# Optimization experiments

Measured on AMD Instinct MI355X. Metric: run time of the kernel, lower is better.

## Reference

```python
import jax, jax.numpy as jnp
import numpy as np

C = 1000      # num_classes
U = 10        # proxies_per_class
D = 512       # feature_dim
B = 4096      # batch
ALPHA = 32.0
DELTA = 0.1


def _l2norm(x, axis=-1):
    return x / jnp.linalg.norm(x, axis=axis, keepdims=True).clip(1e-12)


def setup_inputs() -> dict:
    key = jax.random.key(0)
    k1, k2, k3 = jax.random.split(key, 3)
    features = jax.random.normal(k1, (B, D), dtype=jnp.float32)
    labels = jax.random.randint(k2, (B,), 0, C)
    # proxies are initialized to row-normalized gaussians (as in __init__)
    proxies = _l2norm(jax.random.normal(k3, (C * U, D), dtype=jnp.float32))
    return {"features": features, "labels": labels, "proxies": proxies}


def reference(features, labels, proxies):
    # proxy_class_ids: [C*U], class id of each proxy
    class_ids = jnp.repeat(jnp.arange(C), U)

    x = _l2norm(features)          # [B, D]
    p = _l2norm(proxies)           # [P, D], P = C*U
    sim = x @ p.T                  # [B, P]

    # ---- infer_logits, agg='soft', tau=1 ----
    s = sim.reshape(B, C, U)       # per-class proxy similarities
    w = jax.nn.softmax(s, axis=2)
    logits = jnp.sum(w * s, axis=2)  # [B, C], tau=1 so no extra scaling

    # ---- _compute_proxy_loss (Proxy-Anchor) ----
    sim_t = sim.T                                         # [P, B]
    pos_mask = labels[None, :] == class_ids[:, None]      # [P, B]
    neg_inf = jnp.finfo(jnp.float32).min
    z_pos = jnp.where(pos_mask, -ALPHA * (sim_t - DELTA), neg_inf)
    z_neg = jnp.where(pos_mask, neg_inf, ALPHA * (sim_t + DELTA))
    lse_pos = jax.nn.logsumexp(z_pos, axis=1)             # [P]
    lse_neg = jax.nn.logsumexp(z_neg, axis=1)             # [P]
    pos_term = jax.nn.softplus(lse_pos)
    neg_term = jax.nn.softplus(lse_neg)
    has_pos = pos_mask.any(axis=1)
    pos_loss = jnp.where(has_pos, pos_term, 0.0).sum() / jnp.maximum(
        has_pos.sum(), 1).astype(jnp.float32)
    neg_loss = neg_term.mean()
    proxy_loss = pos_loss + neg_loss

    return logits, proxy_loss
```

## Files before the change

kernel.cpp:

```cpp
#include <hip/hip_runtime.h>
#include <hip/hip_bf16.h>

#define C_CLS   1000
#define U_PX    10
#define D_DIM   512
#define B_BATCH 4096
#define P_PX    (C_CLS * U_PX)
#define ALPHA_F 32.0f
#define DELTA_F 0.1f

#define BM 256
#define BN 80
#define BK 64
#define SIMP 84

#define A_OFF   0
#define B_OFF   32768
#define SMEM_SZ 43008

typedef __attribute__((ext_vector_type(8))) short bf16x8;
typedef __attribute__((ext_vector_type(4))) float f32x4;

typedef __attribute__((address_space(1))) const void gv_t;
typedef __attribute__((address_space(3))) void lv_t;

__device__ __forceinline__ void gload_lds16(const void* g, void* lds) {
    __builtin_amdgcn_global_load_lds((gv_t*)g, (lv_t*)lds, 16, 0, 0);
}

__device__ __forceinline__ unsigned int f2bf(float f) {
    union { float f; unsigned u; } c; c.f = f;
    unsigned u = c.u;
    return (u + 0x7FFF + ((u >> 16) & 1)) >> 16;
}

__global__ __launch_bounds__(256) void norm_rows_kernel(const float* __restrict__ feat,
                                                        const float* __restrict__ prox,
                                                        unsigned int* __restrict__ xout,
                                                        unsigned int* __restrict__ pout) {
    const int wid  = threadIdx.x >> 6;
    const int lane = threadIdx.x & 63;
    int row = blockIdx.x * 4 + wid;
    const float* in;
    unsigned int* out;
    if (row < B_BATCH) { in = feat + (size_t)row * D_DIM;   out = xout + (size_t)row * (D_DIM / 2); }
    else { row -= B_BATCH; in = prox + (size_t)row * D_DIM; out = pout + (size_t)row * (D_DIM / 2); }
    const float4 v0 = reinterpret_cast<const float4*>(in)[lane * 2];
    const float4 v1 = reinterpret_cast<const float4*>(in)[lane * 2 + 1];
    float ss = v0.x*v0.x + v0.y*v0.y + v0.z*v0.z + v0.w*v0.w
             + v1.x*v1.x + v1.y*v1.y + v1.z*v1.z + v1.w*v1.w;
    #pragma unroll
    for (int off = 1; off < 64; off <<= 1) ss += __shfl_xor(ss, off, 64);
    const float inv = 1.0f / fmaxf(sqrtf(ss), 1e-12f);
    uint4 o;
    o.x = f2bf(v0.x * inv) | (f2bf(v0.y * inv) << 16);
    o.y = f2bf(v0.z * inv) | (f2bf(v0.w * inv) << 16);
    o.z = f2bf(v1.x * inv) | (f2bf(v1.y * inv) << 16);
    o.w = f2bf(v1.z * inv) | (f2bf(v1.w * inv) << 16);
    *reinterpret_cast<uint4*>(out + lane * 4) = o;
}

__global__ __launch_bounds__(256, 3) void fused_gemm_kernel(
    const unsigned short* __restrict__ xbf,
    const unsigned short* __restrict__ pbf,
    const int*            __restrict__ labels,
    float*                __restrict__ logits,
    double*               __restrict__ pos_sum,
    double*               __restrict__ neg_sum)
{
    __shared__ __align__(16) char smem[SMEM_SZ];
    __shared__ int lab_lds[BM];

    const int t    = threadIdx.x;
    const int m0   = blockIdx.x * BM;
    const int n0   = blockIdx.y * BN;
    const int wid  = t >> 6;
    const int lane = t & 63;
    const int l15  = lane & 15;
    const int kgrp = lane >> 4;

    if (t < BM) lab_lds[t] = labels[m0 + t];

    const int srow = lane >> 3;
    const int scol = (lane & 7) ^ srow;

    const int koff0 = ((kgrp    ) ^ (l15 & 7)) << 4;
    const int koff1 = ((kgrp + 4) ^ (l15 & 7)) << 4;

    f32x4 acc[4][5];
    #pragma unroll
    for (int m = 0; m < 4; ++m)
        #pragma unroll
        for (int n = 0; n < 5; ++n) acc[m][n] = (f32x4){0.f, 0.f, 0.f, 0.f};

    for (int ks = 0; ks < D_DIM / BK; ++ks) {
        const int kbase = ks * BK;
        #pragma unroll
        for (int c = wid; c < 32; c += 4)
            gload_lds16(xbf + (size_t)(m0 + c * 8 + srow) * D_DIM + kbase + scol * 8,
                        smem + A_OFF + c * 1024);
        for (int c = wid; c < 10; c += 4)
            gload_lds16(pbf + (size_t)(n0 + c * 8 + srow) * D_DIM + kbase + scol * 8,
                        smem + B_OFF + c * 1024);
        __syncthreads();
        #pragma unroll
        for (int kk8 = 0; kk8 < 2; ++kk8) {
            const int koff = kk8 ? koff1 : koff0;
            bf16x8 b[5];
            #pragma unroll
            for (int n = 0; n < 5; ++n)
                b[n] = *reinterpret_cast<const bf16x8*>(smem + B_OFF + (n * 16 + l15) * 128 + koff);
            #pragma unroll
            for (int m = 0; m < 4; ++m) {
                const bf16x8 a = *reinterpret_cast<const bf16x8*>(
                    smem + A_OFF + (wid * 64 + m * 16 + l15) * 128 + koff);
                #pragma unroll
                for (int n = 0; n < 5; ++n)
                    acc[m][n] = __builtin_amdgcn_mfma_f32_16x16x32_bf16(a, b[n], acc[m][n], 0, 0, 0);
            }
        }
        __syncthreads();
    }

    {
        int labv[16];
        #pragma unroll
        for (int m = 0; m < 4; ++m)
            #pragma unroll
            for (int r = 0; r < 4; ++r)
                labv[m * 4 + r] = lab_lds[wid * 64 + m * 16 + kgrp * 4 + r];
        #pragma unroll
        for (int n = 0; n < 5; ++n) {
            const int col = n * 16 + l15;
            const int cls = (n0 + col) / U_PX;
            float pos = 0.f, neg = 0.f;
            #pragma unroll
            for (int m = 0; m < 4; ++m)
                #pragma unroll
                for (int r = 0; r < 4; ++r) {
                    const float s = acc[m][n][r];
                    const bool isp = (labv[m * 4 + r] == cls);
                    const float e = __expf(isp ? (-ALPHA_F * (s - DELTA_F))
                                               : ( ALPHA_F * (s + DELTA_F)));
                    if (isp) pos += e; else neg += e;
                }
            pos += __shfl_xor(pos, 16, 64); pos += __shfl_xor(pos, 32, 64);
            neg += __shfl_xor(neg, 16, 64); neg += __shfl_xor(neg, 32, 64);
            if (lane < 16) {
                atomicAdd(&neg_sum[n0 + col], (double)neg);
                if (pos != 0.f) atomicAdd(&pos_sum[n0 + col], (double)pos);
            }
        }
    }

    float* simw = reinterpret_cast<float*>(smem) + wid * (16 * SIMP);
    #pragma unroll
    for (int m = 0; m < 4; ++m) {
        #pragma unroll
        for (int n = 0; n < 5; ++n)
            #pragma unroll
            for (int r = 0; r < 4; ++r)
                simw[(kgrp * 4 + r) * SIMP + n * 16 + l15] = acc[m][n][r];
        #pragma unroll
        for (int it = 0; it < 2; ++it) {
            const int j   = lane + it * 64;
            const int r   = j >> 3;
            const int c   = j & 7;
            const float* s = simw + r * SIMP + c * U_PX;
            float wsum = 0.f, wssum = 0.f;
            #pragma unroll
            for (int u = 0; u < U_PX; ++u) {
                const float sv = s[u];
                const float e = __expf(sv);
                wsum += e; wssum += e * sv;
            }
            logits[(size_t)(m0 + wid * 64 + m * 16 + r) * C_CLS + (n0 / U_PX + c)] = wssum / wsum;
        }
        __builtin_amdgcn_s_waitcnt(0);
    }
}

__global__ __launch_bounds__(1024) void finalize_kernel(
    const int*    __restrict__ labels,
    const double* __restrict__ pos_sum,
    const double* __restrict__ neg_sum,
    float*        __restrict__ out_loss)
{
    __shared__ int    hist[C_CLS];
    __shared__ double sp[1024], sn[1024];
    __shared__ int    sc[1024];
    const int t = threadIdx.x;
    for (int i = t; i < C_CLS; i += 1024) hist[i] = 0;
    __syncthreads();
    for (int i = t; i < B_BATCH; i += 1024) atomicAdd(&hist[labels[i]], 1);
    __syncthreads();
    double pAcc = 0.0, nAcc = 0.0; int cnt = 0;
    for (int p = t; p < P_PX; p += 1024) {
        nAcc += log1p(neg_sum[p]);
        if (hist[p / U_PX] > 0) { pAcc += log1p(pos_sum[p]); cnt++; }
    }
    sp[t] = pAcc; sn[t] = nAcc; sc[t] = cnt;
    __syncthreads();
    for (int s = 512; s > 0; s >>= 1) {
        if (t < s) { sp[t] += sp[t + s]; sn[t] += sn[t + s]; sc[t] += sc[t + s]; }
        __syncthreads();
    }
    if (t == 0)
        out_loss[0] = (float)(sp[0] / (double)max(sc[0], 1) + sn[0] / (double)P_PX);
}

extern "C" void kernel_launch(void* const* d_in, const int* in_sizes, int n_in,
                              void* d_out, int out_size, void* d_ws, size_t ws_size,
                              hipStream_t stream) {
    const float* features = (const float*)d_in[0];
    const int*   labels   = (const int*)d_in[1];
    const float* proxies  = (const float*)d_in[2];
    float* out = (float*)d_out;

    char* ws = (char*)d_ws;
    unsigned short* xbf = (unsigned short*)ws;
    unsigned short* pbf = (unsigned short*)(ws + (size_t)B_BATCH * D_DIM * 2);
    double* pos_sum = (double*)(ws + (size_t)(B_BATCH + P_PX) * D_DIM * 2);
    double* neg_sum = pos_sum + P_PX;

    hipMemsetAsync(pos_sum, 0, 2 * P_PX * sizeof(double), stream);

    norm_rows_kernel<<<(B_BATCH + P_PX) / 4, 256, 0, stream>>>(
        features, proxies, (unsigned int*)xbf, (unsigned int*)pbf);

    fused_gemm_kernel<<<dim3(B_BATCH / BM, P_PX / BN), 256, 0, stream>>>(
        xbf, pbf, labels, out, pos_sum, neg_sum);

    finalize_kernel<<<1, 1024, 0, stream>>>(labels, pos_sum, neg_sum,
                                            out + (size_t)B_BATCH * C_CLS);
}
```

Baseline: 106.6 us.

## Double-buffer GEMM LDS tiles with smaller blocks and parallelize loss finalize

The fused GEMM kernel now uses 128-row tiles with two waves per block and two LDS buffers, so the global-to-LDS loads for the next K step are issued before the MFMA work on the current one. This is meant to overlap memory traffic with compute and to launch more, smaller blocks. The single-block finalize kernel is replaced by a multi-block partial reduction using wave shuffles and double atomics, followed by a tiny final kernel. The label histogram is dropped in favour of testing whether pos_sum is nonzero, which assumes the exp terms never underflow to zero.

```diff
diff --git a/kernel.cpp b/kernel.cpp
--- a/kernel.cpp
+++ b/kernel.cpp
@@ -9,14 +9,15 @@
 #define ALPHA_F 32.0f
 #define DELTA_F 0.1f
 
-#define BM 256
+#define BM 128
 #define BN 80
 #define BK 64
 #define SIMP 84
 
-#define A_OFF   0
-#define B_OFF   32768
-#define SMEM_SZ 43008
+#define A_OFF      0
+#define B_OFF      16384
+#define BUF_STRIDE 26624
+#define SMEM_SZ    (2 * BUF_STRIDE)
 
 typedef __attribute__((ext_vector_type(8))) short bf16x8;
 typedef __attribute__((ext_vector_type(4))) float f32x4;
@@ -60,7 +61,7 @@
     *reinterpret_cast<uint4*>(out + lane * 4) = o;
 }
 
-__global__ __launch_bounds__(256, 3) void fused_gemm_kernel(
+__global__ __launch_bounds__(128, 3) void fused_gemm_kernel(
     const unsigned short* __restrict__ xbf,
     const unsigned short* __restrict__ pbf,
     const int*            __restrict__ labels,
@@ -79,7 +80,7 @@
     const int l15  = lane & 15;
     const int kgrp = lane >> 4;
 
-    if (t < BM) lab_lds[t] = labels[m0 + t];
+    lab_lds[t] = labels[m0 + t];
 
     const int srow = lane >> 3;
     const int scol = (lane & 7) ^ srow;
@@ -93,27 +94,37 @@
         #pragma unroll
         for (int n = 0; n < 5; ++n) acc[m][n] = (f32x4){0.f, 0.f, 0.f, 0.f};
 
+    #define STAGE(ks_, buf_)                                                            \
+        do {                                                                            \
+            const int kb_ = (ks_) * BK;                                                 \
+            char* base_ = smem + (buf_) * BUF_STRIDE;                                   \
+            _Pragma("unroll")                                                           \
+            for (int c = wid; c < 16; c += 2)                                           \
+                gload_lds16(xbf + (size_t)(m0 + c * 8 + srow) * D_DIM + kb_ + scol * 8, \
+                            base_ + A_OFF + c * 1024);                                  \
+            _Pragma("unroll")                                                           \
+            for (int c = wid; c < 10; c += 2)                                           \
+                gload_lds16(pbf + (size_t)(n0 + c * 8 + srow) * D_DIM + kb_ + scol * 8, \
+                            base_ + B_OFF + c * 1024);                                  \
+        } while (0)
+
+    STAGE(0, 0);
+    __syncthreads();
+
     for (int ks = 0; ks < D_DIM / BK; ++ks) {
-        const int kbase = ks * BK;
-        #pragma unroll
-        for (int c = wid; c < 32; c += 4)
-            gload_lds16(xbf + (size_t)(m0 + c * 8 + srow) * D_DIM + kbase + scol * 8,
-                        smem + A_OFF + c * 1024);
-        for (int c = wid; c < 10; c += 4)
-            gload_lds16(pbf + (size_t)(n0 + c * 8 + srow) * D_DIM + kbase + scol * 8,
-                        smem + B_OFF + c * 1024);
-        __syncthreads();
+        const char* base = smem + (ks & 1) * BUF_STRIDE;
+        if (ks < D_DIM / BK - 1) STAGE(ks + 1, (ks + 1) & 1);
         #pragma unroll
         for (int kk8 = 0; kk8 < 2; ++kk8) {
             const int koff = kk8 ? koff1 : koff0;
             bf16x8 b[5];
             #pragma unroll
             for (int n = 0; n < 5; ++n)
-                b[n] = *reinterpret_cast<const bf16x8*>(smem + B_OFF + (n * 16 + l15) * 128 + koff);
+                b[n] = *reinterpret_cast<const bf16x8*>(smem + (ks & 1) * BUF_STRIDE + B_OFF + (n * 16 + l15) * 128 + koff);
             #pragma unroll
             for (int m = 0; m < 4; ++m) {
                 const bf16x8 a = *reinterpret_cast<const bf16x8*>(
-                    smem + A_OFF + (wid * 64 + m * 16 + l15) * 128 + koff);
+                    base + A_OFF + (wid * 64 + m * 16 + l15) * 128 + koff);
                 #pragma unroll
                 for (int n = 0; n < 5; ++n)
                     acc[m][n] = __builtin_amdgcn_mfma_f32_16x16x32_bf16(a, b[n], acc[m][n], 0, 0, 0);
@@ -180,33 +191,38 @@
     }
 }
 
-__global__ __launch_bounds__(1024) void finalize_kernel(
-    const int*    __restrict__ labels,
+__global__ __launch_bounds__(256) void finalize_partial_kernel(
     const double* __restrict__ pos_sum,
     const double* __restrict__ neg_sum,
-    float*        __restrict__ out_loss)
+    double*       __restrict__ accum)
 {
-    __shared__ int    hist[C_CLS];
-    __shared__ double sp[1024], sn[1024];
-    __shared__ int    sc[1024];
-    const int t = threadIdx.x;
-    for (int i = t; i < C_CLS; i += 1024) hist[i] = 0;
-    __syncthreads();
-    for (int i = t; i < B_BATCH; i += 1024) atomicAdd(&hist[labels[i]], 1);
-    __syncthreads();
-    double pAcc = 0.0, nAcc = 0.0; int cnt = 0;
-    for (int p = t; p < P_PX; p += 1024) {
-        nAcc += log1p(neg_sum[p]);
-        if (hist[p / U_PX] > 0) { pAcc += log1p(pos_sum[p]); cnt++; }
-    }
-    sp[t] = pAcc; sn[t] = nAcc; sc[t] = cnt;
-    __syncthreads();
-    for (int s = 512; s > 0; s >>= 1) {
-        if (t < s) { sp[t] += sp[t + s]; sn[t] += sn[t + s]; sc[t] += sc[t + s]; }
-        __syncthreads();
-    }
-    if (t == 0)
-        out_loss[0] = (float)(sp[0] / (double)max(sc[0], 1) + sn[0] / (double)P_PX);
+    const int p = blockIdx.x * 256 + threadIdx.x;
+    double pv = 0.0, nv = 0.0;
+    int c = 0;
+    if (p < P_PX) {
+        nv = log1p(neg_sum[p]);
+        const double ps = pos_sum[p];
+        if (ps != 0.0) { pv = log1p(ps); c = 1; }
+    }
+    #pragma unroll
+    for (int off = 1; off < 64; off <<= 1) {
+        pv += __shfl_xor(pv, off, 64);
+        nv += __shfl_xor(nv, off, 64);
+        c  += __shfl_xor(c,  off, 64);
+    }
+    if ((threadIdx.x & 63) == 0) {
+        atomicAdd(&accum[0], pv);
+        atomicAdd(&accum[1], nv);
+        atomicAdd((int*)(accum + 2), c);
+    }
+}
+
+__global__ void finalize_final_kernel(const double* __restrict__ accum,
+                                      float* __restrict__ out_loss) {
+    if (threadIdx.x == 0) {
+        const int cnt = *(const int*)(accum + 2);
+        out_loss[0] = (float)(accum[0] / (double)max(cnt, 1) + accum[1] / (double)P_PX);
+    }
 }
 
 extern "C" void kernel_launch(void* const* d_in, const int* in_sizes, int n_in,
@@ -222,15 +238,16 @@
     unsigned short* pbf = (unsigned short*)(ws + (size_t)B_BATCH * D_DIM * 2);
     double* pos_sum = (double*)(ws + (size_t)(B_BATCH + P_PX) * D_DIM * 2);
     double* neg_sum = pos_sum + P_PX;
-
-    hipMemsetAsync(pos_sum, 0, 2 * P_PX * sizeof(double), stream);
+    double* accum   = neg_sum + P_PX;
+
+    hipMemsetAsync(pos_sum, 0, (2 * P_PX + 3) * sizeof(double), stream);
 
     norm_rows_kernel<<<(B_BATCH + P_PX) / 4, 256, 0, stream>>>(
         features, proxies, (unsigned int*)xbf, (unsigned int*)pbf);
 
-    fused_gemm_kernel<<<dim3(B_BATCH / BM, P_PX / BN), 256, 0, stream>>>(
+    fused_gemm_kernel<<<dim3(B_BATCH / BM, P_PX / BN), 128, 0, stream>>>(
         xbf, pbf, labels, out, pos_sum, neg_sum);
 
-    finalize_kernel<<<1, 1024, 0, stream>>>(labels, pos_sum, neg_sum,
-                                            out + (size_t)B_BATCH * C_CLS);
-}
+    finalize_partial_kernel<<<(P_PX + 255) / 256, 256, 0, stream>>>(pos_sum, neg_sum, accum);
+    finalize_final_kernel<<<1, 64, 0, stream>>>(accum, out + (size_t)B_BATCH * C_CLS);
+}
```

New measurement: 131.2 us. +23.1%, slower.
